# Performance work log

Measured on AMD Instinct MI355X. Metric: run time of the kernel, lower is better.

## Reference

```python
import jax, jax.numpy as jnp
import numpy as np

N_NODES = 200000
N_EDGES = 6400000
N_GRAPHS = 128


def setup_inputs() -> dict:
    key = jax.random.key(0)
    k1, k2, k3, k4, k5, k6, k7 = jax.random.split(key, 7)
    x = jax.random.normal(k1, (N_NODES, 1), dtype=jnp.float32)
    edge_index = jax.random.randint(k2, (2, N_EDGES), 0, N_NODES, dtype=jnp.int64)
    batch = jnp.sort(jax.random.randint(k3, (N_NODES,), 0, N_GRAPHS, dtype=jnp.int64))
    # GCNConv parameters (glorot-ish scale)
    W1 = jax.random.normal(k4, (1, 32), dtype=jnp.float32) * (1.0 / np.sqrt(1 + 32))
    b1 = jnp.zeros((32,), dtype=jnp.float32)
    W2 = jax.random.normal(k5, (32, 8), dtype=jnp.float32) * (1.0 / np.sqrt(32 + 8))
    b2 = jnp.zeros((8,), dtype=jnp.float32)
    return {"x": x, "edge_index": edge_index, "batch": batch,
            "W1": W1, "b1": b1, "W2": W2, "b2": b2}


def _gcn_conv(x, src, dst, W, b):
    # x: [N, din] -> [N, dout]; PyG GCNConv: symmetric-normalized A+I aggregation
    h = x @ W                                            # [N, dout]
    deg = jax.ops.segment_sum(jnp.ones_like(dst, h.dtype), dst, num_segments=N_NODES)
    dinv = jnp.where(deg > 0, jax.lax.rsqrt(deg), 0.0)    # [N]
    norm = dinv[src] * dinv[dst]                          # [E+N]
    msg = h[src] * norm[:, None]                          # gather + scale
    out = jax.ops.segment_sum(msg, dst, num_segments=N_NODES)
    return out + b


def reference(x, edge_index, batch, W1, b1, W2, b2):
    loop = jnp.arange(N_NODES, dtype=edge_index.dtype)
    src = jnp.concatenate([edge_index[0], loop])          # add self-loops
    dst = jnp.concatenate([edge_index[1], loop])
    h = _gcn_conv(x, src, dst, W1, b1)
    h = _gcn_conv(h, src, dst, W2, b2)
    # global mean pool over graphs
    sums = jax.ops.segment_sum(h, batch, num_segments=N_GRAPHS)
    cnts = jax.ops.segment_sum(jnp.ones((N_NODES,), h.dtype), batch, num_segments=N_GRAPHS)
    pooled = sums / jnp.maximum(cnts, 1.0)[:, None]       # [G, 8]
    return jax.nn.log_softmax(pooled, axis=1)
```

## Files before the change

### kernel.cpp

```cpp
#include <hip/hip_runtime.h>
#include <math.h>

#define N_NODES 200000
#define N_EDGES 6400000
#define N_GRAPHS 128
#define NI4     (N_EDGES / 4)

#define NBKC  128
#define CBSZ  1568
#define CAP   51712
#define CHK   8000
#define CHK4  (CHK / 4)
#define PBLK  (N_EDGES / CHK)
#define NSUB  8

static __device__ __forceinline__ unsigned bc_of(unsigned n) { return n / (unsigned)CBSZ; }

__global__ void __launch_bounds__(512)
kP1_partition(const int* __restrict__ src, const int* __restrict__ dst,
              unsigned* __restrict__ gcur, unsigned* __restrict__ binned) {
    __shared__ unsigned cnt[NBKC];
    __shared__ unsigned ofs[NBKC];
    __shared__ unsigned cur[NBKC];
    __shared__ unsigned gofs[NBKC];
    __shared__ unsigned stage[CHK];
    const int tid = threadIdx.x;
    if (tid < NBKC) cnt[tid] = 0;
    __syncthreads();

    const int base4 = blockIdx.x * CHK4;
    const int4* s4 = (const int4*)src;
    const int4* d4 = (const int4*)dst;
    int4 sv[4], dv[4];
    bool ok[4];
    #pragma unroll
    for (int k = 0; k < 4; ++k) {
        int e = tid + k * 512;
        ok[k] = (e < CHK4);
        int ec = ok[k] ? e : 0;
        sv[k] = s4[base4 + ec];
        dv[k] = d4[base4 + ec];
    }
    #pragma unroll
    for (int k = 0; k < 4; ++k) {
        if (ok[k]) {
            atomicAdd(&cnt[bc_of((unsigned)dv[k].x)], 1u);
            atomicAdd(&cnt[bc_of((unsigned)dv[k].y)], 1u);
            atomicAdd(&cnt[bc_of((unsigned)dv[k].z)], 1u);
            atomicAdd(&cnt[bc_of((unsigned)dv[k].w)], 1u);
        }
    }
    __syncthreads();
    if (tid < 64) {
        unsigned v0 = cnt[tid];
        unsigned s0 = v0;
        for (int off = 1; off < 64; off <<= 1) {
            unsigned u = __shfl_up(s0, off);
            if (tid >= off) s0 += u;
        }
        unsigned tot0 = __shfl(s0, 63);
        unsigned v1 = cnt[64 + tid];
        unsigned s1 = v1;
        for (int off = 1; off < 64; off <<= 1) {
            unsigned u = __shfl_up(s1, off);
            if (tid >= off) s1 += u;
        }
        ofs[tid] = s0 - v0;
        ofs[64 + tid] = tot0 + s1 - v1;
    }
    __syncthreads();
    if (tid < NBKC) {
        gofs[tid] = atomicAdd(&gcur[tid], cnt[tid]);
        cur[tid] = ofs[tid];
    }
    __syncthreads();
    #pragma unroll
    for (int k = 0; k < 4; ++k) {
        if (ok[k]) {
            unsigned p;
            unsigned b0 = bc_of((unsigned)dv[k].x), l0 = (unsigned)dv[k].x - b0 * CBSZ;
            unsigned b1 = bc_of((unsigned)dv[k].y), l1 = (unsigned)dv[k].y - b1 * CBSZ;
            unsigned b2 = bc_of((unsigned)dv[k].z), l2 = (unsigned)dv[k].z - b2 * CBSZ;
            unsigned b3 = bc_of((unsigned)dv[k].w), l3 = (unsigned)dv[k].w - b3 * CBSZ;
            p = atomicAdd(&cur[b0], 1u); stage[p] = ((unsigned)sv[k].x << 11) | l0;
            p = atomicAdd(&cur[b1], 1u); stage[p] = ((unsigned)sv[k].y << 11) | l1;
            p = atomicAdd(&cur[b2], 1u); stage[p] = ((unsigned)sv[k].z << 11) | l2;
            p = atomicAdd(&cur[b3], 1u); stage[p] = ((unsigned)sv[k].w << 11) | l3;
        }
    }
    __syncthreads();
    const int wave = tid >> 6, lane = tid & 63;
    for (int b = wave; b < NBKC; b += 8) {
        unsigned o = ofs[b];
        unsigned end = (b < NBKC - 1) ? ofs[b + 1] : (unsigned)CHK;
        unsigned c = end - o;
        unsigned gb = gofs[b];
        if (gb >= (unsigned)CAP) continue;
        unsigned avail = (unsigned)CAP - gb;
        if (c > avail) c = avail;
        unsigned gbase = (unsigned)b * CAP + gb;
        for (unsigned i = lane; i < c; i += 64)
            binned[gbase + i] = stage[o + i];
    }
}

__global__ void __launch_bounds__(512)
kB_deg(const unsigned* __restrict__ binned, const unsigned* __restrict__ gcur,
       unsigned* __restrict__ part) {
    __shared__ unsigned bins[CBSZ];
    const int tid = threadIdx.x;
    for (int l = tid; l < CBSZ; l += 512) bins[l] = 0;
    __syncthreads();
    const int bkt = blockIdx.x >> 3, sub = blockIdx.x & 7;
    unsigned cnt = gcur[bkt];
    if (cnt > (unsigned)CAP) cnt = CAP;
    unsigned per = (cnt + NSUB - 1) / NSUB;
    unsigned s = sub * per;
    unsigned e = s + per; if (e > cnt) e = cnt;
    const unsigned base = (unsigned)bkt * CAP;
    unsigned i = base + s + tid;
    const unsigned iend = base + e;
    for (; i + 3u * 512u < iend; i += 4u * 512u) {
        unsigned v0 = binned[i], v1 = binned[i + 512], v2 = binned[i + 1024], v3 = binned[i + 1536];
        atomicAdd(&bins[v0 & 2047u], 1u);
        atomicAdd(&bins[v1 & 2047u], 1u);
        atomicAdd(&bins[v2 & 2047u], 1u);
        atomicAdd(&bins[v3 & 2047u], 1u);
    }
    for (; i < iend; i += 512u) atomicAdd(&bins[binned[i] & 2047u], 1u);
    __syncthreads();
    unsigned* dst = part + (size_t)blockIdx.x * CBSZ;
    for (int l = tid; l < CBSZ; l += 512) dst[l] = bins[l];
}

__global__ void __launch_bounds__(512)
kRedB(const unsigned* __restrict__ part, const float* __restrict__ x,
      const int* __restrict__ batch, float* __restrict__ xd, float2* __restrict__ dstPair) {
    int n = blockIdx.x * 512 + threadIdx.x;
    if (n >= N_NODES) return;
    unsigned b = bc_of((unsigned)n);
    unsigned l = (unsigned)n - b * CBSZ;
    const unsigned* p = part + (size_t)(b * NSUB) * CBSZ + l;
    unsigned d = 0;
    #pragma unroll
    for (int j = 0; j < NSUB; ++j) d += p[(size_t)j * CBSZ];
    float di = rsqrtf((float)d + 1.0f);
    xd[n] = x[n] * di;
    dstPair[n] = make_float2(di, __int_as_float(batch[n]));
}

__global__ void __launch_bounds__(512)
kC_pass1(const unsigned* __restrict__ binned, const unsigned* __restrict__ gcur,
         const float* __restrict__ xd, float* __restrict__ partF) {
    __shared__ float bins[CBSZ];
    const int tid = threadIdx.x;
    for (int l = tid; l < CBSZ; l += 512) bins[l] = 0.0f;
    __syncthreads();
    const int bkt = blockIdx.x >> 3, sub = blockIdx.x & 7;
    unsigned cnt = gcur[bkt];
    if (cnt > (unsigned)CAP) cnt = CAP;
    unsigned per = (cnt + NSUB - 1) / NSUB;
    unsigned s = sub * per;
    unsigned e = s + per; if (e > cnt) e = cnt;
    const unsigned base = (unsigned)bkt * CAP;
    unsigned i = base + s + tid;
    const unsigned iend = base + e;
    for (; i + 3u * 512u < iend; i += 4u * 512u) {
        unsigned v0 = binned[i], v1 = binned[i + 512], v2 = binned[i + 1024], v3 = binned[i + 1536];
        float g0 = xd[v0 >> 11], g1 = xd[v1 >> 11], g2 = xd[v2 >> 11], g3 = xd[v3 >> 11];
        atomicAdd(&bins[v0 & 2047u], g0);
        atomicAdd(&bins[v1 & 2047u], g1);
        atomicAdd(&bins[v2 & 2047u], g2);
        atomicAdd(&bins[v3 & 2047u], g3);
    }
    for (; i < iend; i += 512u) {
        unsigned v = binned[i];
        atomicAdd(&bins[v & 2047u], xd[v >> 11]);
    }
    __syncthreads();
    float* dst = partF + (size_t)blockIdx.x * CBSZ;
    for (int l = tid; l < CBSZ; l += 512) dst[l] = bins[l];
}

__global__ void __launch_bounds__(512)
kRedC(const float* __restrict__ partF, const float* __restrict__ xd,
      const float2* __restrict__ dstPair, float2* __restrict__ srcPair,
      float* __restrict__ gacc) {
    int n = blockIdx.x * 512 + threadIdx.x;
    bool valid = (n < N_NODES);
    float s1 = 0.0f, s0 = 0.0f;
    int g = 0;
    if (valid) {
        unsigned b = bc_of((unsigned)n);
        unsigned l = (unsigned)n - b * CBSZ;
        const float* p = partF + (size_t)(b * NSUB) * CBSZ + l;
        float t = 0.0f;
        #pragma unroll
        for (int j = 0; j < NSUB; ++j) t += p[(size_t)j * CBSZ];
        float2 dp = dstPair[n];
        float di = dp.x;
        g = __float_as_int(dp.y);
        float a = di * (t + xd[n]);
        srcPair[n] = make_float2(a * di, di);
        s1 = a * di * di;
        s0 = di * di;
    }
    int g0 = __shfl(g, 0);
    bool uni = __all(valid && (g == g0));
    if (uni) {
        for (int off = 32; off; off >>= 1) {
            s1 += __shfl_down(s1, off);
            s0 += __shfl_down(s0, off);
        }
        if ((threadIdx.x & 63) == 0) {
            atomicAdd(&gacc[g0], s1);
            atomicAdd(&gacc[N_GRAPHS + g0], s0);
            atomicAdd(&gacc[2 * N_GRAPHS + g0], 64.0f);
        }
    } else if (valid) {
        atomicAdd(&gacc[g], s1);
        atomicAdd(&gacc[N_GRAPHS + g], s0);
        atomicAdd(&gacc[2 * N_GRAPHS + g], 1.0f);
    }
}

#define DBLK  1000
#define DI4   (NI4 / DBLK)

__global__ void __launch_bounds__(512)
kD_edges(const int* __restrict__ src, const int* __restrict__ dst,
         const float2* __restrict__ srcPair, const float2* __restrict__ dstPair,
         float* __restrict__ gacc) {
    __shared__ float wb[N_GRAPHS], zb[N_GRAPHS];
    if (threadIdx.x < N_GRAPHS) { wb[threadIdx.x] = 0.0f; zb[threadIdx.x] = 0.0f; }
    __syncthreads();
    const int base = blockIdx.x * DI4;
    const int4* s4 = (const int4*)src;
    const int4* d4 = (const int4*)dst;
    int4 sv[4], dv[4]; int idx[4];
    #pragma unroll
    for (int k = 0; k < 4; ++k) {
        int i = threadIdx.x + k * 512;
        idx[k] = i;
        int ic = (i < DI4) ? i : (DI4 - 1);
        sv[k] = s4[base + ic];
        dv[k] = d4[base + ic];
    }
    #pragma unroll
    for (int k = 0; k < 4; ++k) {
        float2 sp0 = srcPair[sv[k].x], dp0 = dstPair[dv[k].x];
        float2 sp1 = srcPair[sv[k].y], dp1 = dstPair[dv[k].y];
        float2 sp2 = srcPair[sv[k].z], dp2 = dstPair[dv[k].z];
        float2 sp3 = srcPair[sv[k].w], dp3 = dstPair[dv[k].w];
        if (idx[k] < DI4) {
            int g0 = __float_as_int(dp0.y), g1 = __float_as_int(dp1.y);
            int g2 = __float_as_int(dp2.y), g3 = __float_as_int(dp3.y);
            atomicAdd(&wb[g0], dp0.x * sp0.x); atomicAdd(&zb[g0], dp0.x * sp0.y);
            atomicAdd(&wb[g1], dp1.x * sp1.x); atomicAdd(&zb[g1], dp1.x * sp1.y);
            atomicAdd(&wb[g2], dp2.x * sp2.x); atomicAdd(&zb[g2], dp2.x * sp2.y);
            atomicAdd(&wb[g3], dp3.x * sp3.x); atomicAdd(&zb[g3], dp3.x * sp3.y);
        }
    }
    __syncthreads();
    if (threadIdx.x < N_GRAPHS) {
        atomicAdd(&gacc[threadIdx.x], wb[threadIdx.x]);
        atomicAdd(&gacc[N_GRAPHS + threadIdx.x], zb[threadIdx.x]);
    }
}

__global__ void k_final(const float* __restrict__ gacc,
                        const float* __restrict__ W1, const float* __restrict__ b1,
                        const float* __restrict__ W2, const float* __restrict__ b2,
                        float* __restrict__ out) {
    int g = threadIdx.x;
    if (g >= N_GRAPHS) return;
    float GS1 = gacc[g];
    float GS0 = gacc[N_GRAPHS + g];
    float cnt = gacc[2 * N_GRAPHS + g];
    float denom = fmaxf(cnt, 1.0f);
    float p[8];
    for (int k = 0; k < 8; ++k) {
        float u = 0.0f, v = 0.0f;
        for (int c = 0; c < 32; ++c) {
            u += W1[c] * W2[c * 8 + k];
            v += b1[c] * W2[c * 8 + k];
        }
        p[k] = (u * GS1 + v * GS0 + cnt * b2[k]) / denom;
    }
    float m = p[0];
    for (int k = 1; k < 8; ++k) m = fmaxf(m, p[k]);
    float s = 0.0f;
    for (int k = 0; k < 8; ++k) s += expf(p[k] - m);
    float l = logf(s);
    for (int k = 0; k < 8; ++k) out[g * 8 + k] = p[k] - m - l;
}

__global__ void k_deg(const int* __restrict__ dst, float* __restrict__ deg) {
    const int4* d4 = (const int4*)dst;
    for (int e = blockIdx.x * blockDim.x + threadIdx.x; e < NI4; e += gridDim.x * blockDim.x) {
        int4 d = d4[e];
        atomicAdd(&deg[d.x], 1.0f); atomicAdd(&deg[d.y], 1.0f);
        atomicAdd(&deg[d.z], 1.0f); atomicAdd(&deg[d.w], 1.0f);
    }
}
__global__ void k_dinv(const float* __restrict__ x, float* __restrict__ deg_dinv,
                       float* __restrict__ xd) {
    int i = blockIdx.x * blockDim.x + threadIdx.x;
    if (i < N_NODES) {
        float dinv = rsqrtf(deg_dinv[i] + 1.0f);
        deg_dinv[i] = dinv;
        xd[i] = x[i] * dinv;
    }
}
__global__ void k_pass1(const int* __restrict__ src, const int* __restrict__ dst,
                        const float* __restrict__ xd, float* __restrict__ t) {
    const int4* s4 = (const int4*)src;
    const int4* d4 = (const int4*)dst;
    for (int e = blockIdx.x * blockDim.x + threadIdx.x; e < NI4; e += gridDim.x * blockDim.x) {
        int4 s = s4[e]; int4 d = d4[e];
        atomicAdd(&t[d.x], xd[s.x]); atomicAdd(&t[d.y], xd[s.y]);
        atomicAdd(&t[d.z], xd[s.z]); atomicAdd(&t[d.w], xd[s.w]);
    }
}
__global__ void k_agg1(const float* __restrict__ dinv, const float* __restrict__ xd,
                       float* __restrict__ t, float2* __restrict__ pair) {
    int i = blockIdx.x * blockDim.x + threadIdx.x;
    if (i < N_NODES) {
        float di = dinv[i];
        float a = di * (t[i] + xd[i]);
        t[i] = a;
        pair[i] = make_float2(a * di, di);
    }
}
__global__ void k_pass2(const int* __restrict__ src, const int* __restrict__ dst,
                        const float2* __restrict__ pair,
                        float* __restrict__ s1, float* __restrict__ s0) {
    const int4* s4 = (const int4*)src;
    const int4* d4 = (const int4*)dst;
    for (int e = blockIdx.x * blockDim.x + threadIdx.x; e < NI4; e += gridDim.x * blockDim.x) {
        int4 s = s4[e]; int4 d = d4[e];
        float2 p0 = pair[s.x], p1 = pair[s.y], p2 = pair[s.z], p3 = pair[s.w];
        atomicAdd(&s1[d.x], p0.x); atomicAdd(&s0[d.x], p0.y);
        atomicAdd(&s1[d.y], p1.x); atomicAdd(&s0[d.y], p1.y);
        atomicAdd(&s1[d.z], p2.x); atomicAdd(&s0[d.z], p2.y);
        atomicAdd(&s1[d.w], p3.x); atomicAdd(&s0[d.w], p3.y);
    }
}
__global__ void k_node2(const float* __restrict__ dinv, const float* __restrict__ agg1,
                        const float* __restrict__ s1, const float* __restrict__ s0,
                        const int* __restrict__ batch, float* __restrict__ gacc) {
    int i = blockIdx.x * blockDim.x + threadIdx.x;
    float s1f = 0.0f, s0f = 0.0f; int g = 0;
    bool valid = (i < N_NODES);
    if (valid) {
        float di = dinv[i];
        s1f = di * (s1[i] + agg1[i] * di);
        s0f = di * (s0[i] + di);
        g = batch[i];
    }
    int g0 = __shfl(g, 0);
    bool uni = __all(valid && (g == g0));
    if (uni) {
        for (int off = 32; off; off >>= 1) {
            s1f += __shfl_down(s1f, off);
            s0f += __shfl_down(s0f, off);
        }
        if ((threadIdx.x & 63) == 0) {
            atomicAdd(&gacc[g0], s1f);
            atomicAdd(&gacc[N_GRAPHS + g0], s0f);
            atomicAdd(&gacc[2 * N_GRAPHS + g0], 64.0f);
        }
    } else if (valid) {
        atomicAdd(&gacc[g], s1f);
        atomicAdd(&gacc[N_GRAPHS + g], s0f);
        atomicAdd(&gacc[2 * N_GRAPHS + g], 1.0f);
    }
}


extern "C" void kernel_launch(void* const* d_in, const int* in_sizes, int n_in,
                              void* d_out, int out_size, void* d_ws, size_t ws_size,
                              hipStream_t stream) {
    const float* x     = (const float*)d_in[0];
    const int*   edge  = (const int*)d_in[1];
    const int*   batch = (const int*)d_in[2];
    const float* W1    = (const float*)d_in[3];
    const float* b1    = (const float*)d_in[4];
    const float* W2    = (const float*)d_in[5];
    const float* b2    = (const float*)d_in[6];
    float* out = (float*)d_out;

    const int* src = edge;
    const int* dst = edge + N_EDGES;

    const size_t o_binned  = 0;
    const size_t o_gcur    = o_binned + (size_t)NBKC * CAP;
    const size_t o_part    = o_gcur + NBKC;
    const size_t o_xd      = o_part + (size_t)NBKC * NSUB * CBSZ;
    const size_t o_dstPair = o_xd + N_NODES;
    const size_t o_srcPair = o_dstPair + 2 * (size_t)N_NODES;
    const size_t o_gacc    = o_srcPair + 2 * (size_t)N_NODES;
    const size_t need_u32  = o_gacc + 3 * N_GRAPHS;

    unsigned* ws_u = (unsigned*)d_ws;
    float*    ws_f = (float*)d_ws;

    if (ws_size >= need_u32 * 4) {
        unsigned* binned  = ws_u + o_binned;
        unsigned* gcur    = ws_u + o_gcur;
        unsigned* partU   = ws_u + o_part;
        float*    partF   = (float*)(ws_u + o_part);
        float*    xd      = ws_f + o_xd;
        float2*   dstPair = (float2*)(ws_f + o_dstPair);
        float2*   srcPair = (float2*)(ws_f + o_srcPair);
        float*    gacc    = ws_f + o_gacc;

        hipMemsetAsync(gcur, 0, NBKC * sizeof(unsigned), stream);
        hipMemsetAsync(gacc, 0, 3 * N_GRAPHS * sizeof(float), stream);

        kP1_partition<<<PBLK, 512, 0, stream>>>(src, dst, gcur, binned);
        kB_deg       <<<NBKC * NSUB, 512, 0, stream>>>(binned, gcur, partU);
        kRedB        <<<(N_NODES + 511) / 512, 512, 0, stream>>>(partU, x, batch, xd, dstPair);
        kC_pass1     <<<NBKC * NSUB, 512, 0, stream>>>(binned, gcur, xd, partF);
        kRedC        <<<(N_NODES + 511) / 512, 512, 0, stream>>>(partF, xd, dstPair, srcPair, gacc);
        kD_edges     <<<DBLK, 512, 0, stream>>>(src, dst, srcPair, dstPair, gacc);
        k_final      <<<1, 128, 0, stream>>>(gacc, W1, b1, W2, b2, out);
    } else {
        float* dinv = ws_f;
        float* t    = ws_f + 1 * N_NODES;
        float* s1   = ws_f + 2 * N_NODES;
        float* s0   = ws_f + 3 * N_NODES;
        float* xd   = ws_f + 4 * N_NODES;
        float2* pair = (float2*)(ws_f + 6 * N_NODES);
        float* gacc = ws_f + 8 * N_NODES;

        hipMemsetAsync(ws_f, 0, (size_t)4 * N_NODES * sizeof(float), stream);
        hipMemsetAsync(gacc, 0, (size_t)3 * N_GRAPHS * sizeof(float), stream);

        const int EB = 2048, ET = 256;
        const int NB = (N_NODES + 255) / 256, NT = 256;

        k_deg  <<<EB, ET, 0, stream>>>(dst, dinv);
        k_dinv <<<NB, NT, 0, stream>>>(x, dinv, xd);
        k_pass1<<<EB, ET, 0, stream>>>(src, dst, xd, t);
        k_agg1 <<<NB, NT, 0, stream>>>(dinv, xd, t, pair);
        k_pass2<<<EB, ET, 0, stream>>>(src, dst, pair, s1, s0);
        k_node2<<<NB, NT, 0, stream>>>(dinv, t, s1, s0, batch, gacc);
        k_final<<<1, 128, 0, stream>>>(gacc, W1, b1, W2, b2, out);
    }
}
```

Measured before the change: 207.4 us.

## Replace random-access edge pass with binned second aggregation pass

The final edge pass read raw src/dst edge lists and gathered per-node pairs randomly, then used shared atomics per graph. It is replaced by a second pass over the dst-binned edge array, with bucket-local shared-memory accumulation followed by a per-node reduction. To feed that, pass 1 also accumulates a per-destination sum of dinv[src]. Node data is packed into one float2 (xd, dinv), and batch is read directly. The aim is to swap a scattered, low-locality gather over all edges for bucketed LDS atomics. The cost is an extra partial-sum reduction kernel and doubled LDS atomics in pass 1.

```diff
diff --git a/kernel.cpp b/kernel.cpp
--- a/kernel.cpp
+++ b/kernel.cpp
@@ -12,7 +12,8 @@
 #define CHK   8000
 #define CHK4  (CHK / 4)
 #define PBLK  (N_EDGES / CHK)
-#define NSUB  8
+#define NSUB8 8
+#define NSUB4 4
 
 static __device__ __forceinline__ unsigned bc_of(unsigned n) { return n / (unsigned)CBSZ; }
 
@@ -114,7 +115,7 @@
     const int bkt = blockIdx.x >> 3, sub = blockIdx.x & 7;
     unsigned cnt = gcur[bkt];
     if (cnt > (unsigned)CAP) cnt = CAP;
-    unsigned per = (cnt + NSUB - 1) / NSUB;
+    unsigned per = (cnt + NSUB8 - 1) / NSUB8;
     unsigned s = sub * per;
     unsigned e = s + per; if (e > cnt) e = cnt;
     const unsigned base = (unsigned)bkt * CAP;
@@ -129,37 +130,37 @@
     }
     for (; i < iend; i += 512u) atomicAdd(&bins[binned[i] & 2047u], 1u);
     __syncthreads();
-    unsigned* dst = part + (size_t)blockIdx.x * CBSZ;
-    for (int l = tid; l < CBSZ; l += 512) dst[l] = bins[l];
+    unsigned* dstp = part + (size_t)blockIdx.x * CBSZ;
+    for (int l = tid; l < CBSZ; l += 512) dstp[l] = bins[l];
 }
 
 __global__ void __launch_bounds__(512)
 kRedB(const unsigned* __restrict__ part, const float* __restrict__ x,
-      const int* __restrict__ batch, float* __restrict__ xd, float2* __restrict__ dstPair) {
+      float2* __restrict__ pairBD) {
     int n = blockIdx.x * 512 + threadIdx.x;
     if (n >= N_NODES) return;
     unsigned b = bc_of((unsigned)n);
     unsigned l = (unsigned)n - b * CBSZ;
-    const unsigned* p = part + (size_t)(b * NSUB) * CBSZ + l;
+    const unsigned* p = part + (size_t)(b * NSUB8) * CBSZ + l;
     unsigned d = 0;
     #pragma unroll
-    for (int j = 0; j < NSUB; ++j) d += p[(size_t)j * CBSZ];
+    for (int j = 0; j < NSUB8; ++j) d += p[(size_t)j * CBSZ];
     float di = rsqrtf((float)d + 1.0f);
-    xd[n] = x[n] * di;
-    dstPair[n] = make_float2(di, __int_as_float(batch[n]));
+    pairBD[n] = make_float2(x[n] * di, di);
 }
 
 __global__ void __launch_bounds__(512)
 kC_pass1(const unsigned* __restrict__ binned, const unsigned* __restrict__ gcur,
-         const float* __restrict__ xd, float* __restrict__ partF) {
-    __shared__ float bins[CBSZ];
+         const float2* __restrict__ pairBD, float* __restrict__ partF) {
+    __shared__ float binsT[CBSZ];
+    __shared__ float binsS[CBSZ];
     const int tid = threadIdx.x;
-    for (int l = tid; l < CBSZ; l += 512) bins[l] = 0.0f;
-    __syncthreads();
-    const int bkt = blockIdx.x >> 3, sub = blockIdx.x & 7;
+    for (int l = tid; l < CBSZ; l += 512) { binsT[l] = 0.0f; binsS[l] = 0.0f; }
+    __syncthreads();
+    const int bkt = blockIdx.x >> 2, sub = blockIdx.x & 3;
     unsigned cnt = gcur[bkt];
     if (cnt > (unsigned)CAP) cnt = CAP;
-    unsigned per = (cnt + NSUB - 1) / NSUB;
+    unsigned per = (cnt + NSUB4 - 1) / NSUB4;
     unsigned s = sub * per;
     unsigned e = s + per; if (e > cnt) e = cnt;
     const unsigned base = (unsigned)bkt * CAP;
@@ -167,7 +168,91 @@
     const unsigned iend = base + e;
     for (; i + 3u * 512u < iend; i += 4u * 512u) {
         unsigned v0 = binned[i], v1 = binned[i + 512], v2 = binned[i + 1024], v3 = binned[i + 1536];
-        float g0 = xd[v0 >> 11], g1 = xd[v1 >> 11], g2 = xd[v2 >> 11], g3 = xd[v3 >> 11];
+        float2 p0 = pairBD[v0 >> 11];
+        float2 p1 = pairBD[v1 >> 11];
+        float2 p2 = pairBD[v2 >> 11];
+        float2 p3 = pairBD[v3 >> 11];
+        atomicAdd(&binsT[v0 & 2047u], p0.x); atomicAdd(&binsS[v0 & 2047u], p0.y);
+        atomicAdd(&binsT[v1 & 2047u], p1.x); atomicAdd(&binsS[v1 & 2047u], p1.y);
+        atomicAdd(&binsT[v2 & 2047u], p2.x); atomicAdd(&binsS[v2 & 2047u], p2.y);
+        atomicAdd(&binsT[v3 & 2047u], p3.x); atomicAdd(&binsS[v3 & 2047u], p3.y);
+    }
+    for (; i < iend; i += 512u) {
+        unsigned v = binned[i];
+        float2 p = pairBD[v >> 11];
+        atomicAdd(&binsT[v & 2047u], p.x);
+        atomicAdd(&binsS[v & 2047u], p.y);
+    }
+    __syncthreads();
+    float* dT = partF + (size_t)((bkt * NSUB4 + sub) * 2 + 0) * CBSZ;
+    float* dS = partF + (size_t)((bkt * NSUB4 + sub) * 2 + 1) * CBSZ;
+    for (int l = tid; l < CBSZ; l += 512) { dT[l] = binsT[l]; dS[l] = binsS[l]; }
+}
+
+__global__ void __launch_bounds__(512)
+kRedC(const float* __restrict__ partF, const float2* __restrict__ pairBD,
+      const int* __restrict__ batch, float* __restrict__ adi, float* __restrict__ gacc) {
+    int n = blockIdx.x * 512 + threadIdx.x;
+    bool valid = (n < N_NODES);
+    float c1 = 0.0f, c0 = 0.0f;
+    int g = 0;
+    if (valid) {
+        unsigned b = bc_of((unsigned)n);
+        unsigned l = (unsigned)n - b * CBSZ;
+        const float* p = partF + (size_t)(b * NSUB4) * 2 * CBSZ + l;
+        float t1 = 0.0f, s0 = 0.0f;
+        #pragma unroll
+        for (int j = 0; j < NSUB4; ++j) {
+            t1 += p[(size_t)(2 * j    ) * CBSZ];
+            s0 += p[(size_t)(2 * j + 1) * CBSZ];
+        }
+        float2 pb = pairBD[n];
+        float xd = pb.x, di = pb.y;
+        g = batch[n];
+        float a = di * (t1 + xd);
+        float ad = a * di;
+        adi[n] = ad;
+        c1 = di * ad;
+        c0 = di * (s0 + di);
+    }
+    int g0 = __shfl(g, 0);
+    bool uni = __all(valid && (g == g0));
+    if (uni) {
+        for (int off = 32; off; off >>= 1) {
+            c1 += __shfl_down(c1, off);
+            c0 += __shfl_down(c0, off);
+        }
+        if ((threadIdx.x & 63) == 0) {
+            atomicAdd(&gacc[g0], c1);
+            atomicAdd(&gacc[N_GRAPHS + g0], c0);
+            atomicAdd(&gacc[2 * N_GRAPHS + g0], 64.0f);
+        }
+    } else if (valid) {
+        atomicAdd(&gacc[g], c1);
+        atomicAdd(&gacc[N_GRAPHS + g], c0);
+        atomicAdd(&gacc[2 * N_GRAPHS + g], 1.0f);
+    }
+}
+
+__global__ void __launch_bounds__(512)
+kD2_pass2(const unsigned* __restrict__ binned, const unsigned* __restrict__ gcur,
+          const float* __restrict__ adi, float* __restrict__ partF) {
+    __shared__ float bins[CBSZ];
+    const int tid = threadIdx.x;
+    for (int l = tid; l < CBSZ; l += 512) bins[l] = 0.0f;
+    __syncthreads();
+    const int bkt = blockIdx.x >> 3, sub = blockIdx.x & 7;
+    unsigned cnt = gcur[bkt];
+    if (cnt > (unsigned)CAP) cnt = CAP;
+    unsigned per = (cnt + NSUB8 - 1) / NSUB8;
+    unsigned s = sub * per;
+    unsigned e = s + per; if (e > cnt) e = cnt;
+    const unsigned base = (unsigned)bkt * CAP;
+    unsigned i = base + s + tid;
+    const unsigned iend = base + e;
+    for (; i + 3u * 512u < iend; i += 4u * 512u) {
+        unsigned v0 = binned[i], v1 = binned[i + 512], v2 = binned[i + 1024], v3 = binned[i + 1536];
+        float g0 = adi[v0 >> 11], g1 = adi[v1 >> 11], g2 = adi[v2 >> 11], g3 = adi[v3 >> 11];
         atomicAdd(&bins[v0 & 2047u], g0);
         atomicAdd(&bins[v1 & 2047u], g1);
         atomicAdd(&bins[v2 & 2047u], g2);
@@ -175,96 +260,38 @@
     }
     for (; i < iend; i += 512u) {
         unsigned v = binned[i];
-        atomicAdd(&bins[v & 2047u], xd[v >> 11]);
-    }
-    __syncthreads();
-    float* dst = partF + (size_t)blockIdx.x * CBSZ;
-    for (int l = tid; l < CBSZ; l += 512) dst[l] = bins[l];
-}
-
-__global__ void __launch_bounds__(512)
-kRedC(const float* __restrict__ partF, const float* __restrict__ xd,
-      const float2* __restrict__ dstPair, float2* __restrict__ srcPair,
-      float* __restrict__ gacc) {
+        atomicAdd(&bins[v & 2047u], adi[v >> 11]);
+    }
+    __syncthreads();
+    float* dstp = partF + (size_t)blockIdx.x * CBSZ;
+    for (int l = tid; l < CBSZ; l += 512) dstp[l] = bins[l];
+}
+
+__global__ void __launch_bounds__(512)
+kRedD(const float* __restrict__ partF, const float2* __restrict__ pairBD,
+      const int* __restrict__ batch, float* __restrict__ gacc) {
     int n = blockIdx.x * 512 + threadIdx.x;
     bool valid = (n < N_NODES);
-    float s1 = 0.0f, s0 = 0.0f;
+    float c1 = 0.0f;
     int g = 0;
     if (valid) {
         unsigned b = bc_of((unsigned)n);
         unsigned l = (unsigned)n - b * CBSZ;
-        const float* p = partF + (size_t)(b * NSUB) * CBSZ + l;
-        float t = 0.0f;
+        const float* p = partF + (size_t)(b * NSUB8) * CBSZ + l;
+        float s1 = 0.0f;
         #pragma unroll
-        for (int j = 0; j < NSUB; ++j) t += p[(size_t)j * CBSZ];
-        float2 dp = dstPair[n];
-        float di = dp.x;
-        g = __float_as_int(dp.y);
-        float a = di * (t + xd[n]);
-        srcPair[n] = make_float2(a * di, di);
-        s1 = a * di * di;
-        s0 = di * di;
+        for (int j = 0; j < NSUB8; ++j) s1 += p[(size_t)j * CBSZ];
+        float di = pairBD[n].y;
+        g = batch[n];
+        c1 = di * s1;
     }
     int g0 = __shfl(g, 0);
     bool uni = __all(valid && (g == g0));
     if (uni) {
-        for (int off = 32; off; off >>= 1) {
-            s1 += __shfl_down(s1, off);
-            s0 += __shfl_down(s0, off);
-        }
-        if ((threadIdx.x & 63) == 0) {
-            atomicAdd(&gacc[g0], s1);
-            atomicAdd(&gacc[N_GRAPHS + g0], s0);
-            atomicAdd(&gacc[2 * N_GRAPHS + g0], 64.0f);
-        }
+        for (int off = 32; off; off >>= 1) c1 += __shfl_down(c1, off);
+        if ((threadIdx.x & 63) == 0) atomicAdd(&gacc[g0], c1);
     } else if (valid) {
-        atomicAdd(&gacc[g], s1);
-        atomicAdd(&gacc[N_GRAPHS + g], s0);
-        atomicAdd(&gacc[2 * N_GRAPHS + g], 1.0f);
-    }
-}
-
-#define DBLK  1000
-#define DI4   (NI4 / DBLK)
-
-__global__ void __launch_bounds__(512)
-kD_edges(const int* __restrict__ src, const int* __restrict__ dst,
-         const float2* __restrict__ srcPair, const float2* __restrict__ dstPair,
-         float* __restrict__ gacc) {
-    __shared__ float wb[N_GRAPHS], zb[N_GRAPHS];
-    if (threadIdx.x < N_GRAPHS) { wb[threadIdx.x] = 0.0f; zb[threadIdx.x] = 0.0f; }
-    __syncthreads();
-    const int base = blockIdx.x * DI4;
-    const int4* s4 = (const int4*)src;
-    const int4* d4 = (const int4*)dst;
-    int4 sv[4], dv[4]; int idx[4];
-    #pragma unroll
-    for (int k = 0; k < 4; ++k) {
-        int i = threadIdx.x + k * 512;
-        idx[k] = i;
-        int ic = (i < DI4) ? i : (DI4 - 1);
-        sv[k] = s4[base + ic];
-        dv[k] = d4[base + ic];
-    }
-    #pragma unroll
-    for (int k = 0; k < 4; ++k) {
-        float2 sp0 = srcPair[sv[k].x], dp0 = dstPair[dv[k].x];
-        float2 sp1 = srcPair[sv[k].y], dp1 = dstPair[dv[k].y];
-        float2 sp2 = srcPair[sv[k].z], dp2 = dstPair[dv[k].z];
-        float2 sp3 = srcPair[sv[k].w], dp3 = dstPair[dv[k].w];
-        if (idx[k] < DI4) {
-            int g0 = __float_as_int(dp0.y), g1 = __float_as_int(dp1.y);
-            int g2 = __float_as_int(dp2.y), g3 = __float_as_int(dp3.y);
-            atomicAdd(&wb[g0], dp0.x * sp0.x); atomicAdd(&zb[g0], dp0.x * sp0.y);
-            atomicAdd(&wb[g1], dp1.x * sp1.x); atomicAdd(&zb[g1], dp1.x * sp1.y);
-            atomicAdd(&wb[g2], dp2.x * sp2.x); atomicAdd(&zb[g2], dp2.x * sp2.y);
-            atomicAdd(&wb[g3], dp3.x * sp3.x); atomicAdd(&zb[g3], dp3.x * sp3.y);
-        }
-    }
-    __syncthreads();
-    if (threadIdx.x < N_GRAPHS) {
-        atomicAdd(&gacc[threadIdx.x], wb[threadIdx.x]);
-        atomicAdd(&gacc[N_GRAPHS + threadIdx.x], zb[threadIdx.x]);
+        atomicAdd(&gacc[g], c1);
     }
 }
 
@@ -393,14 +420,13 @@
     const int* src = edge;
     const int* dst = edge + N_EDGES;
 
-    const size_t o_binned  = 0;
-    const size_t o_gcur    = o_binned + (size_t)NBKC * CAP;
-    const size_t o_part    = o_gcur + NBKC;
-    const size_t o_xd      = o_part + (size_t)NBKC * NSUB * CBSZ;
-    const size_t o_dstPair = o_xd + N_NODES;
-    const size_t o_srcPair = o_dstPair + 2 * (size_t)N_NODES;
-    const size_t o_gacc    = o_srcPair + 2 * (size_t)N_NODES;
-    const size_t need_u32  = o_gacc + 3 * N_GRAPHS;
+    const size_t o_binned = 0;
+    const size_t o_gcur   = o_binned + (size_t)NBKC * CAP;
+    const size_t o_part   = o_gcur + NBKC;
+    const size_t o_pairBD = o_part + (size_t)NBKC * NSUB8 * CBSZ;
+    const size_t o_adi    = o_pairBD + 2 * (size_t)N_NODES;
+    const size_t o_gacc   = o_adi + N_NODES;
+    const size_t need_u32 = o_gacc + 3 * N_GRAPHS;
 
     unsigned* ws_u = (unsigned*)d_ws;
     float*    ws_f = (float*)d_ws;
@@ -410,20 +436,20 @@
         unsigned* gcur    = ws_u + o_gcur;
         unsigned* partU   = ws_u + o_part;
         float*    partF   = (float*)(ws_u + o_part);
-        float*    xd      = ws_f + o_xd;
-        float2*   dstPair = (float2*)(ws_f + o_dstPair);
-        float2*   srcPair = (float2*)(ws_f + o_srcPair);
+        float2*   pairBD  = (float2*)(ws_f + o_pairBD);
+        float*    adi     = ws_f + o_adi;
         float*    gacc    = ws_f + o_gacc;
 
         hipMemsetAsync(gcur, 0, NBKC * sizeof(unsigned), stream);
         hipMemsetAsync(gacc, 0, 3 * N_GRAPHS * sizeof(float), stream);
 
         kP1_partition<<<PBLK, 512, 0, stream>>>(src, dst, gcur, binned);
-        kB_deg       <<<NBKC * NSUB, 512, 0, stream>>>(binned, gcur, partU);
-        kRedB        <<<(N_NODES + 511) / 512, 512, 0, stream>>>(partU, x, batch, xd, dstPair);
-        kC_pass1     <<<NBKC * NSUB, 512, 0, stream>>>(binned, gcur, xd, partF);
-        kRedC        <<<(N_NODES + 511) / 512, 512, 0, stream>>>(partF, xd, dstPair, srcPair, gacc);
-        kD_edges     <<<DBLK, 512, 0, stream>>>(src, dst, srcPair, dstPair, gacc);
+        kB_deg       <<<NBKC * NSUB8, 512, 0, stream>>>(binned, gcur, partU);
+        kRedB        <<<(N_NODES + 511) / 512, 512, 0, stream>>>(partU, x, pairBD);
+        kC_pass1     <<<NBKC * NSUB4, 512, 0, stream>>>(binned, gcur, pairBD, partF);
+        kRedC        <<<(N_NODES + 511) / 512, 512, 0, stream>>>(partF, pairBD, batch, adi, gacc);
+        kD2_pass2    <<<NBKC * NSUB8, 512, 0, stream>>>(binned, gcur, adi, partF);
+        kRedD        <<<(N_NODES + 511) / 512, 512, 0, stream>>>(partF, pairBD, batch, gacc);
         k_final      <<<1, 128, 0, stream>>>(gacc, W1, b1, W2, b2, out);
     } else {
         float* dinv = ws_f;
```

Measured after the change: 238.3 us. 1.15x slower.
